# Kernel tuning notes

Hardware: AMD Instinct MI355X
Metric: run time of the kernel (lower is better)

Reference implementation:

```python
import jax, jax.numpy as jnp
import numpy as np

C = 1.0                     # curvature
BALL_EPS = 1e-3             # pmath.project boundary epsilon (float32)
ATANH_CLAMP = 1.0 - 1e-5    # artanh argument clamp
MIN_DENOM = 1e-15
INIT_NORM = 0.4             # prototype_init_norm


def setup_inputs() -> dict:
    key = jax.random.key(0)
    kx, kr, kp = jax.random.split(key, 3)
    N, K, D = 16384, 128, 64
    # Points strictly inside the Poincare ball: random direction * radius in [0, 0.8)
    v = jax.random.normal(kx, (N, D), dtype=jnp.float32)
    v = v / jnp.maximum(jnp.linalg.norm(v, axis=-1, keepdims=True), 1e-8)
    r = jax.random.uniform(kr, (N, 1), dtype=jnp.float32) * 0.8
    x = v * r
    # Prototypes: unit directions scaled to init norm (as in __init__)
    p = jax.random.normal(kp, (K, D), dtype=jnp.float32)
    p = p / jnp.maximum(jnp.linalg.norm(p, axis=-1, keepdims=True), 1e-8)
    prototypes = p * INIT_NORM
    return {"x": x, "prototypes": prototypes}


def _project_ball(p, c):
    # pmath.project: clamp norm to (1 - eps) / sqrt(c)
    maxnorm = (1.0 - BALL_EPS) / jnp.sqrt(c)
    n = jnp.maximum(jnp.linalg.norm(p, axis=-1, keepdims=True), 1e-15)
    return p * jnp.minimum(1.0, maxnorm / n)


def reference(x, prototypes):
    c = jnp.float32(C)
    sqrt_c = jnp.sqrt(c)
    p = _project_ball(prototypes, c)            # (K, D)

    xe = x[:, None, :]                          # (N, 1, D)
    pe = p[None, :, :]                          # (1, K, D)
    x2 = jnp.sum(xe * xe, axis=-1, keepdims=True)   # (N, 1, 1)
    p2 = jnp.sum(pe * pe, axis=-1, keepdims=True)   # (1, K, 1)
    xy = jnp.sum(xe * pe, axis=-1, keepdims=True)   # (N, K, 1)

    # mobius_add(-x, p) with u = -x: <u,p> = -<x,p>, ||u||^2 = ||x||^2
    num = (1.0 - 2.0 * c * xy + c * p2) * (-xe) + (1.0 - c * x2) * pe  # (N,K,D)
    den = 1.0 - 2.0 * c * xy + (c * c) * x2 * p2                       # (N,K,1)
    ma = num / jnp.maximum(den, MIN_DENOM)

    ma_norm = jnp.sqrt(jnp.sum(ma * ma, axis=-1))        # (N, K)
    z = jnp.clip(sqrt_c * ma_norm, 0.0, ATANH_CLAMP)
    dist = (2.0 / sqrt_c) * jnp.arctanh(z)               # geodesic distance
    return -(dist * dist)                                # logits (N, K)
```

## Files before the change

### kernel.cpp

```cpp
#include <hip/hip_runtime.h>
#include <math.h>


#define K_PROTO 128
#define D_DIM   64
#define BN      16
#define STRIDE  68

__global__ __launch_bounds__(256, 4) void geodesic_kernel(
    const float* __restrict__ x,
    const float* __restrict__ p,
    float* __restrict__ out)
{
    __shared__ __align__(16) float ps[K_PROTO * STRIDE];
    __shared__ __align__(16) float xs[BN * STRIDE];
    __shared__ float sx2[BN];
    __shared__ float sp2[K_PROTO];
    __shared__ float ssc[K_PROTO];

    const int t  = threadIdx.x;
    const int n0 = blockIdx.x * BN;

    {
        int r  = t >> 4;
        int c4 = (t & 15) << 2;
        float4 v = *(const float4*)(x + (size_t)(n0 + r) * D_DIM + c4);
        *(float4*)(&xs[r * STRIDE + c4]) = v;
    }
    #pragma unroll
    for (int it = 0; it < 8; ++it) {
        int idx = t + 256 * it;
        int r   = idx >> 4;
        int c4  = (idx & 15) << 2;
        float4 v = *(const float4*)(p + (size_t)r * D_DIM + c4);
        *(float4*)(&ps[r * STRIDE + c4]) = v;
    }
    __syncthreads();

    if (t < K_PROTO) {
        float s2 = 0.f;
        #pragma unroll
        for (int i = 0; i < 16; ++i) {
            float4 v = *(const float4*)(&ps[t * STRIDE + 4 * i]);
            s2 += v.x * v.x + v.y * v.y + v.z * v.z + v.w * v.w;
        }
        float nrm = fmaxf(sqrtf(s2), 1e-15f);
        float sc  = fminf(1.0f, 0.999f / nrm);
        ssc[t] = sc;
        sp2[t] = s2 * sc * sc;
    } else if (t < K_PROTO + BN) {
        int r = t - K_PROTO;
        float s2 = 0.f;
        #pragma unroll
        for (int i = 0; i < 16; ++i) {
            float4 v = *(const float4*)(&xs[r * STRIDE + 4 * i]);
            s2 += v.x * v.x + v.y * v.y + v.z * v.z + v.w * v.w;
        }
        sx2[r] = s2;
    }
    __syncthreads();

    const int tn = t & 15;
    const int kg = t >> 4;

    float acc[8];
    #pragma unroll
    for (int m = 0; m < 8; ++m) acc[m] = 0.f;

    #pragma unroll 2
    for (int i = 0; i < 16; ++i) {
        float4 xv = *(const float4*)(&xs[tn * STRIDE + 4 * i]);
        #pragma unroll
        for (int m = 0; m < 8; ++m) {
            float4 pv = *(const float4*)(&ps[(kg + 16 * m) * STRIDE + 4 * i]);
            acc[m] += xv.x * pv.x + xv.y * pv.y + xv.z * pv.z + xv.w * pv.w;
        }
    }

    const float x2 = sx2[tn];
    const float b  = 1.0f - x2;
    float* orow = out + (size_t)(n0 + tn) * K_PROTO;

    #pragma unroll
    for (int m = 0; m < 8; ++m) {
        int   k   = kg + 16 * m;
        float xy  = acc[m] * ssc[k];
        float p2  = sp2[k];
        float a   = 1.0f - 2.0f * xy + p2;
        float den = fmaxf(1.0f - 2.0f * xy + x2 * p2, 1e-15f);
        float num2 = fmaxf(a * a * x2 - 2.0f * a * b * xy + b * b * p2, 0.0f);
        float z   = fminf(__fdividef(sqrtf(num2), den), 1.0f - 1e-05f);
        float l   = __logf(__fdividef(1.0f + z, 1.0f - z));
        orow[k] = -(l * l);
    }
}

extern "C" void kernel_launch(void* const* d_in, const int* in_sizes, int n_in,
                              void* d_out, int out_size, void* d_ws, size_t ws_size,
                              hipStream_t stream) {
    const float* x = (const float*)d_in[0];
    const float* p = (const float*)d_in[1];
    float* out = (float*)d_out;

    dim3 grid(16384 / BN);
    dim3 block(256);
    hipLaunchKernelGGL(geodesic_kernel, grid, block, 0, stream, x, p, out);
}
```

Baseline: 69.41 us.

## Compute dot products with split-bf16 MFMA and retile over N and K

```diff
diff --git a/kernel.cpp b/kernel.cpp
--- a/kernel.cpp
+++ b/kernel.cpp
@@ -2,96 +2,142 @@
 #include <math.h>
 
 
+typedef __attribute__((ext_vector_type(8))) short bf16x8;
+typedef __attribute__((ext_vector_type(4))) float f32x4;
+
 #define K_PROTO 128
 #define D_DIM   64
-#define BN      16
-#define STRIDE  68
+#define BN      64
+#define BK      64
+#define PAD     72
 
-__global__ __launch_bounds__(256, 4) void geodesic_kernel(
+__device__ __forceinline__ unsigned f2bfbits(float f) {
+    unsigned u = __float_as_uint(f);
+    return (u + 0x7fffu + ((u >> 16) & 1u)) >> 16;
+}
+__device__ __forceinline__ void cvt1(float f, short* h, short* l) {
+    unsigned hb = f2bfbits(f);
+    float lo = f - __uint_as_float(hb << 16);
+    *h = (short)hb;
+    *l = (short)f2bfbits(lo);
+}
+__device__ __forceinline__ void cvt8(float4 v0, float4 v1, bf16x8* h8, bf16x8* l8) {
+    short hs, ls;
+    cvt1(v0.x,&hs,&ls); (*h8)[0]=hs; (*l8)[0]=ls;
+    cvt1(v0.y,&hs,&ls); (*h8)[1]=hs; (*l8)[1]=ls;
+    cvt1(v0.z,&hs,&ls); (*h8)[2]=hs; (*l8)[2]=ls;
+    cvt1(v0.w,&hs,&ls); (*h8)[3]=hs; (*l8)[3]=ls;
+    cvt1(v1.x,&hs,&ls); (*h8)[4]=hs; (*l8)[4]=ls;
+    cvt1(v1.y,&hs,&ls); (*h8)[5]=hs; (*l8)[5]=ls;
+    cvt1(v1.z,&hs,&ls); (*h8)[6]=hs; (*l8)[6]=ls;
+    cvt1(v1.w,&hs,&ls); (*h8)[7]=hs; (*l8)[7]=ls;
+}
+
+__global__ __launch_bounds__(256) void geodesic_mfma(
     const float* __restrict__ x,
     const float* __restrict__ p,
     float* __restrict__ out)
 {
-    __shared__ __align__(16) float ps[K_PROTO * STRIDE];
-    __shared__ __align__(16) float xs[BN * STRIDE];
+    __shared__ __align__(16) short ph[BK * PAD];
+    __shared__ __align__(16) short pl[BK * PAD];
+    __shared__ float sp2[BK];
+    __shared__ float ssc[BK];
     __shared__ float sx2[BN];
-    __shared__ float sp2[K_PROTO];
-    __shared__ float ssc[K_PROTO];
 
     const int t  = threadIdx.x;
-    const int n0 = blockIdx.x * BN;
+    const int nb = (int)blockIdx.x >> 1;
+    const int kb = (int)blockIdx.x & 1;
+    const int n0 = nb * BN;
+    const int k0 = kb * BK;
 
     {
-        int r  = t >> 4;
-        int c4 = (t & 15) << 2;
-        float4 v = *(const float4*)(x + (size_t)(n0 + r) * D_DIM + c4);
-        *(float4*)(&xs[r * STRIDE + c4]) = v;
+        const int row = t >> 2;
+        const int dq  = (t & 3) << 4;
+        const float* pr = p + (size_t)(k0 + row) * D_DIM + dq;
+        #pragma unroll
+        for (int hh = 0; hh < 2; ++hh) {
+            float4 v0 = *(const float4*)(pr + 8 * hh);
+            float4 v1 = *(const float4*)(pr + 8 * hh + 4);
+            bf16x8 h8, l8;
+            cvt8(v0, v1, &h8, &l8);
+            *(bf16x8*)(&ph[row * PAD + dq + 8 * hh]) = h8;
+            *(bf16x8*)(&pl[row * PAD + dq + 8 * hh]) = l8;
+        }
     }
-    #pragma unroll
-    for (int it = 0; it < 8; ++it) {
-        int idx = t + 256 * it;
-        int r   = idx >> 4;
-        int c4  = (idx & 15) << 2;
-        float4 v = *(const float4*)(p + (size_t)r * D_DIM + c4);
-        *(float4*)(&ps[r * STRIDE + c4]) = v;
-    }
-    __syncthreads();
 
-    if (t < K_PROTO) {
+    if (t < BK) {
+        const float* pr = p + (size_t)(k0 + t) * D_DIM;
         float s2 = 0.f;
         #pragma unroll
         for (int i = 0; i < 16; ++i) {
-            float4 v = *(const float4*)(&ps[t * STRIDE + 4 * i]);
-            s2 += v.x * v.x + v.y * v.y + v.z * v.z + v.w * v.w;
+            float4 v = *(const float4*)(pr + 4 * i);
+            s2 += v.x*v.x + v.y*v.y + v.z*v.z + v.w*v.w;
         }
         float nrm = fmaxf(sqrtf(s2), 1e-15f);
         float sc  = fminf(1.0f, 0.999f / nrm);
         ssc[t] = sc;
         sp2[t] = s2 * sc * sc;
-    } else if (t < K_PROTO + BN) {
-        int r = t - K_PROTO;
+    } else if (t < BK + BN) {
+        const int r = t - BK;
+        const float* xr = x + (size_t)(n0 + r) * D_DIM;
         float s2 = 0.f;
         #pragma unroll
         for (int i = 0; i < 16; ++i) {
-            float4 v = *(const float4*)(&xs[r * STRIDE + 4 * i]);
-            s2 += v.x * v.x + v.y * v.y + v.z * v.z + v.w * v.w;
+            float4 v = *(const float4*)(xr + 4 * i);
+            s2 += v.x*v.x + v.y*v.y + v.z*v.z + v.w*v.w;
         }
         sx2[r] = s2;
     }
     __syncthreads();
 
-    const int tn = t & 15;
-    const int kg = t >> 4;
+    const int w    = t >> 6;
+    const int lane = t & 63;
+    const int q    = lane >> 4;
+    const int m16  = lane & 15;
 
-    float acc[8];
-    #pragma unroll
-    for (int m = 0; m < 8; ++m) acc[m] = 0.f;
-
-    #pragma unroll 2
-    for (int i = 0; i < 16; ++i) {
-        float4 xv = *(const float4*)(&xs[tn * STRIDE + 4 * i]);
-        #pragma unroll
-        for (int m = 0; m < 8; ++m) {
-            float4 pv = *(const float4*)(&ps[(kg + 16 * m) * STRIDE + 4 * i]);
-            acc[m] += xv.x * pv.x + xv.y * pv.y + xv.z * pv.z + xv.w * pv.w;
-        }
+    bf16x8 xh0, xl0, xh1, xl1;
+    {
+        const float* xr = x + (size_t)(n0 + w * 16 + m16) * D_DIM + q * 8;
+        float4 a0 = *(const float4*)(xr);
+        float4 a1 = *(const float4*)(xr + 4);
+        float4 b0 = *(const float4*)(xr + 32);
+        float4 b1 = *(const float4*)(xr + 36);
+        cvt8(a0, a1, &xh0, &xl0);
+        cvt8(b0, b1, &xh1, &xl1);
     }
 
-    const float x2 = sx2[tn];
-    const float b  = 1.0f - x2;
-    float* orow = out + (size_t)(n0 + tn) * K_PROTO;
+    #pragma unroll
+    for (int kt = 0; kt < 4; ++kt) {
+        const int klocal = kt * 16 + m16;
+        const int off    = klocal * PAD + q * 8;
+        bf16x8 bh0 = *(const bf16x8*)(&ph[off]);
+        bf16x8 bh1 = *(const bf16x8*)(&ph[off + 32]);
+        bf16x8 bl0 = *(const bf16x8*)(&pl[off]);
+        bf16x8 bl1 = *(const bf16x8*)(&pl[off + 32]);
 
-    #pragma unroll
-    for (int m = 0; m < 8; ++m) {
-        int   k   = kg + 16 * m;
-        float xy  = acc[m] * ssc[k];
-        float p2  = sp2[k];
-        float a   = 1.0f - 2.0f * xy + p2;
-        float den = fmaxf(1.0f - 2.0f * xy + x2 * p2, 1e-15f);
-        float num2 = fmaxf(a * a * x2 - 2.0f * a * b * xy + b * b * p2, 0.0f);
-        float z   = fminf(__fdividef(sqrtf(num2), den), 1.0f - 1e-05f);
-        float l   = __logf(__fdividef(1.0f + z, 1.0f - z));
-        orow[k] = -(l * l);
+        f32x4 acc = {0.f, 0.f, 0.f, 0.f};
+        acc = __builtin_amdgcn_mfma_f32_16x16x32_bf16(xh0, bh0, acc, 0, 0, 0);
+        acc = __builtin_amdgcn_mfma_f32_16x16x32_bf16(xh1, bh1, acc, 0, 0, 0);
+        acc = __builtin_amdgcn_mfma_f32_16x16x32_bf16(xh0, bl0, acc, 0, 0, 0);
+        acc = __builtin_amdgcn_mfma_f32_16x16x32_bf16(xh1, bl1, acc, 0, 0, 0);
+        acc = __builtin_amdgcn_mfma_f32_16x16x32_bf16(xl0, bh0, acc, 0, 0, 0);
+        acc = __builtin_amdgcn_mfma_f32_16x16x32_bf16(xl1, bh1, acc, 0, 0, 0);
+
+        const float scv = ssc[klocal];
+        const float p2  = sp2[klocal];
+        #pragma unroll
+        for (int r = 0; r < 4; ++r) {
+            const int rl  = w * 16 + q * 4 + r;
+            const float x2 = sx2[rl];
+            const float xy = acc[r] * scv;
+            const float aa = 1.0f - 2.0f * xy + p2;
+            const float bb = 1.0f - x2;
+            const float den = fmaxf(1.0f - 2.0f * xy + x2 * p2, 1e-15f);
+            const float n2 = fmaxf(aa*aa*x2 - 2.0f*aa*bb*xy + bb*bb*p2, 0.0f);
+            const float s  = fminf(sqrtf(n2), 0.99999f * den);
+            const float l  = __logf(__fdividef(den + s, den - s));
+            out[(size_t)(n0 + rl) * K_PROTO + k0 + klocal] = -(l * l);
+        }
     }
 }
 
@@ -102,7 +148,7 @@
     const float* p = (const float*)d_in[1];
     float* out = (float*)d_out;
 
-    dim3 grid(16384 / BN);
+    dim3 grid((16384 / BN) * (K_PROTO / BK));
     dim3 block(256);
-    hipLaunchKernelGGL(geodesic_kernel, grid, block, 0, stream, x, p, out);
+    hipLaunchKernelGGL(geodesic_mfma, grid, block, 0, stream, x, p, out);
 }
```

Result: faster. 64.42 us (-7.2%).
